# Optimization experiments

Measured on AMD Instinct MI355X. Metric: run time of the kernel, lower is better.

Reference implementation:

```python
import jax, jax.numpy as jnp
import numpy as np
import math

B, L, D, H = 2, 2048, 1024, 16
DK = D // H


def setup_inputs() -> dict:
    key = jax.random.key(0)
    ks = jax.random.split(key, 11)
    s = 1.0 / math.sqrt(D)
    inp = {
        "query": jax.random.normal(ks[0], (B, L, D), jnp.float32),
        "key": jax.random.normal(ks[1], (B, L, D), jnp.float32),
        "value": jax.random.normal(ks[2], (B, L, D), jnp.float32),
        # mask == True (==1) means masked-out; causal mask over future positions
        "mask": jnp.triu(jnp.ones((L, L), dtype=bool), k=1),
        "Wq": jax.random.normal(ks[3], (D, D), jnp.float32) * s,
        "bq": jnp.zeros((D,), jnp.float32),
        "Wk": jax.random.normal(ks[4], (D, D), jnp.float32) * s,
        "bk": jnp.zeros((D,), jnp.float32),
        "Wv": jax.random.normal(ks[5], (D, D), jnp.float32) * s,
        "bv": jnp.zeros((D,), jnp.float32),
        "Wo": jax.random.normal(ks[6], (D, D), jnp.float32) * s,
        "bo": jnp.zeros((D,), jnp.float32),
    }
    return inp


def reference(query, key, value, mask, Wq, bq, Wk, bk, Wv, bv, Wo, bo):
    # Linear projections, then split heads: [B, L, D] -> [B, H, L, DK]
    def proj(x, W, b):
        return (x @ W.T + b).reshape(B, -1, H, DK).transpose(0, 2, 1, 3)

    Q = proj(query, Wq, bq)
    K = proj(key, Wk, bk)
    V = proj(value, Wv, bv)

    scale = 1.0 / math.sqrt(DK)
    scores = jnp.einsum("bhqd,bhkd->bhqk", Q, K) * scale  # [B,H,Lq,Lk]
    scores = jnp.where(mask, -jnp.inf, scores)
    attn = jax.nn.softmax(scores, axis=-1)  # dropout p=0 (eval mode)
    out = jnp.einsum("bhqk,bhkd->bhqd", attn, V)
    out = out.transpose(0, 2, 1, 3).reshape(B, -1, D)  # merge heads
    return out @ Wo.T + bo
```

## Files before the change

### kernel.cpp

```cpp
#include <hip/hip_runtime.h>
#include <hip/hip_bf16.h>
#include <math.h>

#define NL 2048
#define ND 1024

typedef __attribute__((ext_vector_type(8))) __bf16 bf16x8;
typedef __attribute__((ext_vector_type(4))) float f32x4;
typedef __attribute__((ext_vector_type(16))) float f32x16;
typedef __attribute__((ext_vector_type(4))) short short4v;
typedef __attribute__((ext_vector_type(2))) unsigned uint2v;
typedef __attribute__((ext_vector_type(4))) unsigned uint4v;

__device__ __forceinline__ short f2bf(float f) {
    union { float f; unsigned u; } v; v.f = f;
    unsigned u = v.u;
    u += 0x7FFF + ((u >> 16) & 1);
    return (short)(u >> 16);
}

__device__ __forceinline__ unsigned cvtpk2(float lo, float hi) {
    unsigned r;
    asm("v_cvt_pk_bf16_f32 %0, %1, %2" : "=v"(r) : "v"(lo), "v"(hi));
    return r;
}

__device__ __forceinline__ void gload16(const short* g, short* l) {
    __builtin_amdgcn_global_load_lds(
        (const __attribute__((address_space(1))) void*)g,
        (__attribute__((address_space(3))) void*)l, 16, 0, 0);
}

__global__ __launch_bounds__(256) void cvt_f32_bf16_3(const float* __restrict__ a,
                                                      const float* __restrict__ b,
                                                      const float* __restrict__ c,
                                                      short* __restrict__ dst, int per) {
    const float* src = blockIdx.y == 0 ? a : blockIdx.y == 1 ? b : c;
    short* d = dst + (size_t)blockIdx.y * per;
    int i = (blockIdx.x * 256 + threadIdx.x) * 8;
    if (i < per) {
        f32x4 v0 = *(const f32x4*)&src[i];
        f32x4 v1 = *(const f32x4*)&src[i + 4];
        uint4v u = { cvtpk2(v0[0], v0[1]), cvtpk2(v0[2], v0[3]),
                     cvtpk2(v1[0], v1[1]), cvtpk2(v1[2], v1[3]) };
        *(uint4v*)&d[i] = u;
    }
}

__global__ __launch_bounds__(256) void gemm_qkv(
    const float* __restrict__ Xq, const float* __restrict__ Xk, const float* __restrict__ Xv,
    const short* __restrict__ Wqb, const short* __restrict__ Wkb, const short* __restrict__ Wvb,
    const float* __restrict__ bq, const float* __restrict__ bk, const float* __restrict__ bv,
    short* __restrict__ oq, short* __restrict__ ok, short* __restrict__ ov) {
    __shared__ alignas(16) short As[2][128 * 32];
    __shared__ alignas(16) short Bs[2][128 * 32];

    const int bid  = blockIdx.x;
    const int xcd  = bid & 7, slot = bid >> 3;
    const int panel = xcd * 12 + (slot >> 3);
    const int z    = panel >> 5;
    const int m0   = (panel & 31) * 128;
    const int n0   = (slot & 7) * 128;

    const float* X  = z == 0 ? Xq : z == 1 ? Xk : Xv;
    const short* Wb = z == 0 ? Wqb : z == 1 ? Wkb : Wvb;
    const float* bi = z == 0 ? bq : z == 1 ? bk : bv;
    short* outp     = z == 0 ? oq : z == 1 ? ok : ov;
    const float scl = z == 0 ? 0.125f * 1.44269504088896f : 1.0f;

    const int tid = threadIdx.x, lane = tid & 63, w = tid >> 6;
    const int wr = w >> 1, wc = w & 1, lr = lane >> 4, lc = lane & 15;

    const short* gB = &Wb[(n0 + w * 16 + (lane >> 2)) * 1024 + (lane & 3) * 8];
    const float* gA = &X[(m0 + (tid >> 3)) * 1024 + (tid & 7) * 4];
    const int arow = tid >> 3, acol = (tid & 7) * 4;

    f32x4 acc[4][4] = {};
    f32x4 av[4];

    #pragma unroll
    for (int p = 0; p < 4; ++p) av[p] = *(const f32x4*)&gA[p * 32 * 1024];
    gload16(gB, &Bs[0][w * 512]);
    gload16(gB + 64 * 1024, &Bs[0][w * 512 + 2048]);
    #pragma unroll
    for (int p = 0; p < 4; ++p) {
        uint2v uu = { cvtpk2(av[p][0], av[p][1]), cvtpk2(av[p][2], av[p][3]) };
        *(uint2v*)&As[0][(p * 32 + arow) * 32 + acol] = uu;
    }
    __syncthreads();

    int cur = 0;
    for (int t = 0; t < 32; ++t) {
        const int k1 = (t + 1) * 32;
        if (t < 31) {
            #pragma unroll
            for (int p = 0; p < 4; ++p)
                av[p] = *(const f32x4*)&gA[p * 32 * 1024 + k1];
            gload16(gB + k1, &Bs[cur ^ 1][w * 512]);
            gload16(gB + 64 * 1024 + k1, &Bs[cur ^ 1][w * 512 + 2048]);
        }

        bf16x8 a[4], b[4];
        #pragma unroll
        for (int mt = 0; mt < 4; ++mt)
            a[mt] = *(const bf16x8*)&As[cur][(wr * 64 + mt * 16 + lc) * 32 + lr * 8];
        #pragma unroll
        for (int nt = 0; nt < 4; ++nt)
            b[nt] = *(const bf16x8*)&Bs[cur][(wc * 64 + nt * 16 + lc) * 32 + lr * 8];
        __builtin_amdgcn_s_setprio(1);
        #pragma unroll
        for (int mt = 0; mt < 4; ++mt)
            #pragma unroll
            for (int nt = 0; nt < 4; ++nt)
                acc[mt][nt] = __builtin_amdgcn_mfma_f32_16x16x32_bf16(
                    a[mt], b[nt], acc[mt][nt], 0, 0, 0);
        __builtin_amdgcn_s_setprio(0);

        if (t < 31) {
            #pragma unroll
            for (int p = 0; p < 4; ++p) {
                uint2v uu = { cvtpk2(av[p][0], av[p][1]), cvtpk2(av[p][2], av[p][3]) };
                *(uint2v*)&As[cur ^ 1][(p * 32 + arow) * 32 + acol] = uu;
            }
        }
        __syncthreads();
        cur ^= 1;
    }

    #pragma unroll
    for (int mt = 0; mt < 4; ++mt)
        #pragma unroll
        for (int nt = 0; nt < 4; ++nt)
            #pragma unroll
            for (int r = 0; r < 4; ++r) {
                int grow = m0 + wr * 64 + mt * 16 + lr * 4 + r;
                int gcol = n0 + wc * 64 + nt * 16 + lc;
                float val = (acc[mt][nt][r] + bi[gcol]) * scl;
                int bh = (grow >> 11) * 16 + (gcol >> 6);
                int q  = grow & 2047;
                int dk = gcol & 63;
                size_t addr;
                if (z == 2)
                    addr = (size_t)bh * 131072 + (size_t)(q >> 6) * 4096 +
                           ((q >> 4) & 3) * 1024 + (dk >> 5) * 512 +
                           ((q >> 3) & 1) * 256 + (dk & 31) * 8 + (q & 7);
                else
                    addr = (size_t)bh * 131072 + (size_t)(q >> 5) * 2048 +
                           (dk >> 4) * 512 + ((dk >> 3) & 1) * 256 +
                           (q & 31) * 8 + (dk & 7);
                outp[addr] = f2bf(val);
            }
}

__global__ __launch_bounds__(256) void gemm_out(const short* __restrict__ Abf,
                                                const short* __restrict__ Wob,
                                                const float* __restrict__ bo,
                                                float* __restrict__ out) {
    __shared__ alignas(16) short As[2][128 * 32];
    __shared__ alignas(16) short Bs[2][128 * 32];

    const int bid = blockIdx.x;
    const int xcd = bid & 7, slot = bid >> 3;
    const int m0  = (xcd * 4 + (slot >> 3)) * 128;
    const int n0  = (slot & 7) * 128;

    const int tid = threadIdx.x, lane = tid & 63, w = tid >> 6;
    const int wr = w >> 1, wc = w & 1, lr = lane >> 4, lc = lane & 15;

    const short* gA = &Abf[(m0 + w * 16 + (lane >> 2)) * 1024 + (lane & 3) * 8];
    const short* gB = &Wob[(n0 + w * 16 + (lane >> 2)) * 1024 + (lane & 3) * 8];

    f32x4 acc[4][4] = {};

    gload16(gA, &As[0][w * 512]);
    gload16(gA + 64 * 1024, &As[0][w * 512 + 2048]);
    gload16(gB, &Bs[0][w * 512]);
    gload16(gB + 64 * 1024, &Bs[0][w * 512 + 2048]);
    __syncthreads();

    int cur = 0;
    for (int t = 0; t < 32; ++t) {
        const int k1 = (t + 1) * 32;
        if (t < 31) {
            gload16(gA + k1, &As[cur ^ 1][w * 512]);
            gload16(gA + 64 * 1024 + k1, &As[cur ^ 1][w * 512 + 2048]);
            gload16(gB + k1, &Bs[cur ^ 1][w * 512]);
            gload16(gB + 64 * 1024 + k1, &Bs[cur ^ 1][w * 512 + 2048]);
        }

        bf16x8 a[4], b[4];
        #pragma unroll
        for (int mt = 0; mt < 4; ++mt)
            a[mt] = *(const bf16x8*)&As[cur][(wr * 64 + mt * 16 + lc) * 32 + lr * 8];
        #pragma unroll
        for (int nt = 0; nt < 4; ++nt)
            b[nt] = *(const bf16x8*)&Bs[cur][(wc * 64 + nt * 16 + lc) * 32 + lr * 8];
        __builtin_amdgcn_s_setprio(1);
        #pragma unroll
        for (int mt = 0; mt < 4; ++mt)
            #pragma unroll
            for (int nt = 0; nt < 4; ++nt)
                acc[mt][nt] = __builtin_amdgcn_mfma_f32_16x16x32_bf16(
                    a[mt], b[nt], acc[mt][nt], 0, 0, 0);
        __builtin_amdgcn_s_setprio(0);
        __syncthreads();
        cur ^= 1;
    }

    #pragma unroll
    for (int mt = 0; mt < 4; ++mt)
        #pragma unroll
        for (int nt = 0; nt < 4; ++nt)
            #pragma unroll
            for (int r = 0; r < 4; ++r) {
                int grow = m0 + wr * 64 + mt * 16 + lr * 4 + r;
                int gcol = n0 + wc * 64 + nt * 16 + lc;
                out[grow * 1024 + gcol] = acc[mt][nt][r] + bo[gcol];
            }
}

__global__ __launch_bounds__(128, 3) void flash_attn(const short* __restrict__ Q,
                                                     const short* __restrict__ K,
                                                     const short* __restrict__ Vt,
                                                     short* __restrict__ AO) {
    __shared__ float mrg[64][49];

    const int tid  = threadIdx.x;
    const int lane = tid & 63;
    const int w    = tid >> 6;
    const int ql   = lane & 31;
    const int hi   = lane >> 5;

    const int bid  = blockIdx.x;
    const int xcd  = bid & 7;
    const int idx  = bid >> 3;
    const int bh   = xcd * 4 + (idx & 3);
    const int t    = 63 - (idx >> 2);
    const int q0   = t * 32;
    const int qa   = q0 + ql;
    const int nkb  = (t >> 1) + 1;
    const int nkb2 = nkb >> 1;
    const int kb_lo = w == 0 ? 0 : nkb2;
    const int kb_hi = w == 0 ? nkb2 : nkb;

    const short* Qp = Q  + (size_t)bh * 131072 + (size_t)t * 2048 + lane * 8;
    const short* Kp = K  + (size_t)bh * 131072 + lane * 8;
    const short* Vp = Vt + (size_t)bh * 131072 + lane * 8;

    bf16x8 qf[4];
    #pragma unroll
    for (int ks = 0; ks < 4; ++ks)
        qf[ks] = *(const bf16x8*)&Qp[ks * 512];

    f32x16 ot0 = {}, ot1 = {}, lacc = {};

    for (int kb = kb_lo; kb < kb_hi; ++kb) {
        bf16x8 kf[8];
        #pragma unroll
        for (int ks = 0; ks < 4; ++ks) {
            kf[2 * ks]     = *(const bf16x8*)&Kp[(size_t)(2 * kb) * 2048 + ks * 512];
            kf[2 * ks + 1] = *(const bf16x8*)&Kp[(size_t)(2 * kb + 1) * 2048 + ks * 512];
        }

        f32x16 st0 = {}, st1 = {};
        __builtin_amdgcn_s_setprio(1);
        #pragma unroll
        for (int ks = 0; ks < 4; ++ks) {
            st0 = __builtin_amdgcn_mfma_f32_32x32x16_bf16(kf[2 * ks],     qf[ks], st0, 0, 0, 0);
            st1 = __builtin_amdgcn_mfma_f32_32x32x16_bf16(kf[2 * ks + 1], qf[ks], st1, 0, 0, 0);
        }
        __builtin_amdgcn_s_setprio(0);

        bf16x8 vf[8];
        #pragma unroll
        for (int ks = 0; ks < 4; ++ks) {
            vf[2 * ks]     = *(const bf16x8*)&Vp[(size_t)kb * 4096 + ks * 1024];
            vf[2 * ks + 1] = *(const bf16x8*)&Vp[(size_t)kb * 4096 + ks * 1024 + 512];
        }

        if (kb == nkb - 1) {
            const int kv0 = kb * 64;
            #pragma unroll
            for (int r = 0; r < 16; ++r) {
                const int cr = (r & 3) + 8 * (r >> 2) + 4 * hi;
                if (kv0 + cr > qa)      st0[r] = -3.0e38f;
                if (kv0 + 32 + cr > qa) st1[r] = -3.0e38f;
            }
        }

        #pragma unroll
        for (int r = 0; r < 16; ++r) {
            st0[r] = exp2f(st0[r]);
            st1[r] = exp2f(st1[r]);
            lacc[r] += st0[r] + st1[r];
        }

        bf16x8 pf[4];
        #pragma unroll
        for (int blk = 0; blk < 2; ++blk) {
            const f32x16 s = blk ? st1 : st0;
            #pragma unroll
            for (int pks = 0; pks < 2; ++pks) {
                const int b = pks * 8;
                unsigned xa = cvtpk2(s[b + 0], s[b + 1]);
                unsigned xb = cvtpk2(s[b + 2], s[b + 3]);
                unsigned ya = cvtpk2(s[b + 4], s[b + 5]);
                unsigned yb = cvtpk2(s[b + 6], s[b + 7]);
                uint2v s0 = __builtin_amdgcn_permlane32_swap(xa, ya, false, false);
                uint2v s1 = __builtin_amdgcn_permlane32_swap(xb, yb, false, false);
                union { unsigned u[4]; bf16x8 v; } pu;
                pu.u[0] = s0[0]; pu.u[1] = s1[0]; pu.u[2] = s0[1]; pu.u[3] = s1[1];
                pf[blk * 2 + pks] = pu.v;
            }
        }

        __builtin_amdgcn_s_setprio(1);
        #pragma unroll
        for (int ks = 0; ks < 4; ++ks) {
            ot0 = __builtin_amdgcn_mfma_f32_32x32x16_bf16(vf[2 * ks],     pf[ks], ot0, 0, 0, 0);
            ot1 = __builtin_amdgcn_mfma_f32_32x32x16_bf16(vf[2 * ks + 1], pf[ks], ot1, 0, 0, 0);
        }
        __builtin_amdgcn_s_setprio(0);
    }

    if (w == 0) {
        #pragma unroll
        for (int r = 0; r < 16; ++r) {
            mrg[lane][r]      = ot0[r];
            mrg[lane][16 + r] = ot1[r];
            mrg[lane][32 + r] = lacc[r];
        }
    }
    __syncthreads();
    if (w == 1) {
        #pragma unroll
        for (int r = 0; r < 16; ++r) {
            ot0[r]  += mrg[lane][r];
            ot1[r]  += mrg[lane][16 + r];
            lacc[r] += mrg[lane][32 + r];
        }
        float sm[16];
        #pragma unroll
        for (int r = 0; r < 16; ++r) sm[r] = lacc[r];
        #pragma unroll
        for (int s = 8; s > 0; s >>= 1)
            #pragma unroll
            for (int i = 0; i < s; ++i) sm[i] += sm[i + s];
        const float l = sm[0] + __shfl_xor(sm[0], 32);
        const float inv = 1.f / l;

        const int b_ = bh >> 4, h_ = bh & 15;
        short* aoRow = AO + ((size_t)(b_ * NL + qa)) * ND + h_ * 64;
        #pragma unroll
        for (int db = 0; db < 2; ++db) {
            const f32x16 o = db ? ot1 : ot0;
            #pragma unroll
            for (int g = 0; g < 4; ++g) {
                short4v sv;
                #pragma unroll
                for (int i = 0; i < 4; ++i) sv[i] = f2bf(o[g * 4 + i] * inv);
                *(short4v*)&aoRow[db * 32 + g * 8 + 4 * hi] = sv;
            }
        }
    }
}

extern "C" void kernel_launch(void* const* d_in, const int* in_sizes, int n_in,
                              void* d_out, int out_size, void* d_ws, size_t ws_size,
                              hipStream_t stream) {
    const float* query = (const float*)d_in[0];
    const float* key   = (const float*)d_in[1];
    const float* value = (const float*)d_in[2];
    const float* Wq = (const float*)d_in[4];
    const float* bq = (const float*)d_in[5];
    const float* Wk = (const float*)d_in[6];
    const float* bk = (const float*)d_in[7];
    const float* Wv = (const float*)d_in[8];
    const float* bv = (const float*)d_in[9];
    const float* Wo = (const float*)d_in[10];
    const float* bo = (const float*)d_in[11];

    short* ws    = (short*)d_ws;
    short* q_ws  = ws;
    short* k_ws  = ws + (4 << 20);
    short* vt_ws = ws + (8 << 20);
    short* wbf   = ws + (12 << 20);
    short* ao_ws = ws + (12 << 20);
    short* wobf  = ws;

    cvt_f32_bf16_3<<<dim3(512, 3), 256, 0, stream>>>(Wq, Wk, Wv, wbf, 1 << 20);
    gemm_qkv<<<dim3(768), 256, 0, stream>>>(
        query, key, value,
        wbf, wbf + (1 << 20), wbf + (2 << 20),
        bq, bk, bv, q_ws, k_ws, vt_ws);
    flash_attn<<<dim3(2048), dim3(128), 0, stream>>>(q_ws, k_ws, vt_ws, ao_ws);
    cvt_f32_bf16_3<<<dim3(512, 1), 256, 0, stream>>>(Wo, Wo, Wo, wobf, 1 << 20);
    gemm_out<<<dim3(256), 256, 0, stream>>>(ao_ws, wobf, bo, (float*)d_out);
}
```

Before: 119.6 us.

## Deepen GEMM pipelines to triple/quad buffering with one barrier per k-step

The QKV projection GEMM moves from double to triple buffering and keeps two fp32 A prefetches in flight, using explicit vmcnt waits and a single raw s_barrier per k-step. The output GEMM moves to a four-stage LDS ring with loads issued two tiles ahead, also with one barrier per iteration. Both aim to hide global-load latency and drop the second __syncthreads per step. In exchange they use more LDS per block, which may reduce occupancy, and rely on hand-counted waitcnt values being correct.

```diff
diff --git a/kernel.cpp b/kernel.cpp
--- a/kernel.cpp
+++ b/kernel.cpp
@@ -52,8 +52,8 @@
     const short* __restrict__ Wqb, const short* __restrict__ Wkb, const short* __restrict__ Wvb,
     const float* __restrict__ bq, const float* __restrict__ bk, const float* __restrict__ bv,
     short* __restrict__ oq, short* __restrict__ ok, short* __restrict__ ov) {
-    __shared__ alignas(16) short As[2][128 * 32];
-    __shared__ alignas(16) short Bs[2][128 * 32];
+    __shared__ alignas(16) short As[3][4096];
+    __shared__ alignas(16) short Bs[3][4096];
 
     const int bid  = blockIdx.x;
     const int xcd  = bid & 7, slot = bid >> 3;
@@ -76,55 +76,109 @@
     const int arow = tid >> 3, acol = (tid & 7) * 4;
 
     f32x4 acc[4][4] = {};
-    f32x4 av[4];
-
-    #pragma unroll
-    for (int p = 0; p < 4; ++p) av[p] = *(const f32x4*)&gA[p * 32 * 1024];
+    f32x4 avE[4], avO[4];
+
+    #pragma unroll
+    for (int p = 0; p < 4; ++p) avE[p] = *(const f32x4*)&gA[p * 32768];
+    #pragma unroll
+    for (int p = 0; p < 4; ++p) avO[p] = *(const f32x4*)&gA[p * 32768 + 32];
     gload16(gB, &Bs[0][w * 512]);
-    gload16(gB + 64 * 1024, &Bs[0][w * 512 + 2048]);
+    gload16(gB + 65536, &Bs[0][w * 512 + 2048]);
     #pragma unroll
     for (int p = 0; p < 4; ++p) {
-        uint2v uu = { cvtpk2(av[p][0], av[p][1]), cvtpk2(av[p][2], av[p][3]) };
+        uint2v uu = { cvtpk2(avE[p][0], avE[p][1]), cvtpk2(avE[p][2], avE[p][3]) };
         *(uint2v*)&As[0][(p * 32 + arow) * 32 + acol] = uu;
     }
-    __syncthreads();
-
-    int cur = 0;
-    for (int t = 0; t < 32; ++t) {
-        const int k1 = (t + 1) * 32;
-        if (t < 31) {
-            #pragma unroll
-            for (int p = 0; p < 4; ++p)
-                av[p] = *(const f32x4*)&gA[p * 32 * 1024 + k1];
-            gload16(gB + k1, &Bs[cur ^ 1][w * 512]);
-            gload16(gB + 64 * 1024 + k1, &Bs[cur ^ 1][w * 512 + 2048]);
-        }
-
+
+#define QKV_STEP(T, RD, WT, AVL, AVW)                                          \
+    {                                                                          \
+        const int k2 = ((T) + 2) * 32, k1 = ((T) + 1) * 32;                    \
+        _Pragma("unroll")                                                      \
+        for (int p = 0; p < 4; ++p)                                            \
+            AVL[p] = *(const f32x4*)&gA[p * 32768 + k2];                       \
+        gload16(gB + k1, &Bs[WT][w * 512]);                                    \
+        gload16(gB + 65536 + k1, &Bs[WT][w * 512 + 2048]);                     \
+        asm volatile("s_waitcnt vmcnt(6)" ::: "memory");                       \
+        _Pragma("unroll")                                                      \
+        for (int p = 0; p < 4; ++p) {                                          \
+            uint2v uu = { cvtpk2(AVW[p][0], AVW[p][1]),                        \
+                          cvtpk2(AVW[p][2], AVW[p][3]) };                      \
+            *(uint2v*)&As[WT][(p * 32 + arow) * 32 + acol] = uu;               \
+        }                                                                      \
+        asm volatile("s_waitcnt lgkmcnt(0)" ::: "memory");                     \
+        __builtin_amdgcn_s_barrier();                                          \
+        asm volatile("" ::: "memory");                                         \
+        bf16x8 a[4], b[4];                                                     \
+        _Pragma("unroll")                                                      \
+        for (int mt = 0; mt < 4; ++mt)                                         \
+            a[mt] = *(const bf16x8*)&As[RD][(wr * 64 + mt * 16 + lc) * 32 + lr * 8]; \
+        _Pragma("unroll")                                                      \
+        for (int nt = 0; nt < 4; ++nt)                                         \
+            b[nt] = *(const bf16x8*)&Bs[RD][(wc * 64 + nt * 16 + lc) * 32 + lr * 8]; \
+        __builtin_amdgcn_s_setprio(1);                                         \
+        _Pragma("unroll")                                                      \
+        for (int mt = 0; mt < 4; ++mt)                                         \
+            _Pragma("unroll")                                                  \
+            for (int nt = 0; nt < 4; ++nt)                                     \
+                acc[mt][nt] = __builtin_amdgcn_mfma_f32_16x16x32_bf16(         \
+                    a[mt], b[nt], acc[mt][nt], 0, 0, 0);                       \
+        __builtin_amdgcn_s_setprio(0);                                         \
+    }
+
+    int rd = 0;
+    for (int t = 0; t < 30; t += 2) {
+        const int wt0 = rd + 1 == 3 ? 0 : rd + 1;
+        QKV_STEP(t, rd, wt0, avE, avO);
+        const int rd1 = wt0;
+        const int wt1 = rd1 + 1 == 3 ? 0 : rd1 + 1;
+        QKV_STEP(t + 1, rd1, wt1, avO, avE);
+        rd = wt1;
+    }
+#undef QKV_STEP
+
+    {
+        gload16(gB + 31 * 32, &Bs[1][w * 512]);
+        gload16(gB + 65536 + 31 * 32, &Bs[1][w * 512 + 2048]);
+        asm volatile("s_waitcnt vmcnt(2)" ::: "memory");
+        #pragma unroll
+        for (int p = 0; p < 4; ++p) {
+            uint2v uu = { cvtpk2(avO[p][0], avO[p][1]), cvtpk2(avO[p][2], avO[p][3]) };
+            *(uint2v*)&As[1][(p * 32 + arow) * 32 + acol] = uu;
+        }
+        asm volatile("s_waitcnt lgkmcnt(0)" ::: "memory");
+        __builtin_amdgcn_s_barrier();
+        asm volatile("" ::: "memory");
         bf16x8 a[4], b[4];
         #pragma unroll
         for (int mt = 0; mt < 4; ++mt)
-            a[mt] = *(const bf16x8*)&As[cur][(wr * 64 + mt * 16 + lc) * 32 + lr * 8];
-        #pragma unroll
-        for (int nt = 0; nt < 4; ++nt)
-            b[nt] = *(const bf16x8*)&Bs[cur][(wc * 64 + nt * 16 + lc) * 32 + lr * 8];
-        __builtin_amdgcn_s_setprio(1);
+            a[mt] = *(const bf16x8*)&As[0][(wr * 64 + mt * 16 + lc) * 32 + lr * 8];
+        #pragma unroll
+        for (int nt = 0; nt < 4; ++nt)
+            b[nt] = *(const bf16x8*)&Bs[0][(wc * 64 + nt * 16 + lc) * 32 + lr * 8];
         #pragma unroll
         for (int mt = 0; mt < 4; ++mt)
             #pragma unroll
             for (int nt = 0; nt < 4; ++nt)
                 acc[mt][nt] = __builtin_amdgcn_mfma_f32_16x16x32_bf16(
                     a[mt], b[nt], acc[mt][nt], 0, 0, 0);
-        __builtin_amdgcn_s_setprio(0);
-
-        if (t < 31) {
-            #pragma unroll
-            for (int p = 0; p < 4; ++p) {
-                uint2v uu = { cvtpk2(av[p][0], av[p][1]), cvtpk2(av[p][2], av[p][3]) };
-                *(uint2v*)&As[cur ^ 1][(p * 32 + arow) * 32 + acol] = uu;
-            }
-        }
-        __syncthreads();
-        cur ^= 1;
+    }
+    {
+        asm volatile("s_waitcnt vmcnt(0)" ::: "memory");
+        __builtin_amdgcn_s_barrier();
+        asm volatile("" ::: "memory");
+        bf16x8 a[4], b[4];
+        #pragma unroll
+        for (int mt = 0; mt < 4; ++mt)
+            a[mt] = *(const bf16x8*)&As[1][(wr * 64 + mt * 16 + lc) * 32 + lr * 8];
+        #pragma unroll
+        for (int nt = 0; nt < 4; ++nt)
+            b[nt] = *(const bf16x8*)&Bs[1][(wc * 64 + nt * 16 + lc) * 32 + lr * 8];
+        #pragma unroll
+        for (int mt = 0; mt < 4; ++mt)
+            #pragma unroll
+            for (int nt = 0; nt < 4; ++nt)
+                acc[mt][nt] = __builtin_amdgcn_mfma_f32_16x16x32_bf16(
+                    a[mt], b[nt], acc[mt][nt], 0, 0, 0);
     }
 
     #pragma unroll
@@ -156,8 +210,8 @@
                                                 const short* __restrict__ Wob,
                                                 const float* __restrict__ bo,
                                                 float* __restrict__ out) {
-    __shared__ alignas(16) short As[2][128 * 32];
-    __shared__ alignas(16) short Bs[2][128 * 32];
+    __shared__ alignas(16) short As[4][4096];
+    __shared__ alignas(16) short Bs[4][4096];
 
     const int bid = blockIdx.x;
     const int xcd = bid & 7, slot = bid >> 3;
@@ -172,29 +226,33 @@
 
     f32x4 acc[4][4] = {};
 
-    gload16(gA, &As[0][w * 512]);
-    gload16(gA + 64 * 1024, &As[0][w * 512 + 2048]);
-    gload16(gB, &Bs[0][w * 512]);
-    gload16(gB + 64 * 1024, &Bs[0][w * 512 + 2048]);
-    __syncthreads();
-
-    int cur = 0;
-    for (int t = 0; t < 32; ++t) {
-        const int k1 = (t + 1) * 32;
-        if (t < 31) {
-            gload16(gA + k1, &As[cur ^ 1][w * 512]);
-            gload16(gA + 64 * 1024 + k1, &As[cur ^ 1][w * 512 + 2048]);
-            gload16(gB + k1, &Bs[cur ^ 1][w * 512]);
-            gload16(gB + 64 * 1024 + k1, &Bs[cur ^ 1][w * 512 + 2048]);
-        }
+    gload16(gA,         &As[0][w * 512]);
+    gload16(gA + 65536, &As[0][w * 512 + 2048]);
+    gload16(gB,         &Bs[0][w * 512]);
+    gload16(gB + 65536, &Bs[0][w * 512 + 2048]);
+    gload16(gA + 32,         &As[1][w * 512]);
+    gload16(gA + 65536 + 32, &As[1][w * 512 + 2048]);
+    gload16(gB + 32,         &Bs[1][w * 512]);
+    gload16(gB + 65536 + 32, &Bs[1][w * 512 + 2048]);
+
+    for (int t = 0; t < 30; ++t) {
+        const int ws_ = (t + 2) & 3, rd = t & 3;
+        const int k2 = (t + 2) * 32;
+        gload16(gA + k2,         &As[ws_][w * 512]);
+        gload16(gA + 65536 + k2, &As[ws_][w * 512 + 2048]);
+        gload16(gB + k2,         &Bs[ws_][w * 512]);
+        gload16(gB + 65536 + k2, &Bs[ws_][w * 512 + 2048]);
+        asm volatile("s_waitcnt vmcnt(8)" ::: "memory");
+        __builtin_amdgcn_s_barrier();
+        asm volatile("" ::: "memory");
 
         bf16x8 a[4], b[4];
         #pragma unroll
         for (int mt = 0; mt < 4; ++mt)
-            a[mt] = *(const bf16x8*)&As[cur][(wr * 64 + mt * 16 + lc) * 32 + lr * 8];
-        #pragma unroll
-        for (int nt = 0; nt < 4; ++nt)
-            b[nt] = *(const bf16x8*)&Bs[cur][(wc * 64 + nt * 16 + lc) * 32 + lr * 8];
+            a[mt] = *(const bf16x8*)&As[rd][(wr * 64 + mt * 16 + lc) * 32 + lr * 8];
+        #pragma unroll
+        for (int nt = 0; nt < 4; ++nt)
+            b[nt] = *(const bf16x8*)&Bs[rd][(wc * 64 + nt * 16 + lc) * 32 + lr * 8];
         __builtin_amdgcn_s_setprio(1);
         #pragma unroll
         for (int mt = 0; mt < 4; ++mt)
@@ -203,8 +261,27 @@
                 acc[mt][nt] = __builtin_amdgcn_mfma_f32_16x16x32_bf16(
                     a[mt], b[nt], acc[mt][nt], 0, 0, 0);
         __builtin_amdgcn_s_setprio(0);
-        __syncthreads();
-        cur ^= 1;
+    }
+    #pragma unroll
+    for (int pt = 0; pt < 2; ++pt) {
+        if (pt == 0) asm volatile("s_waitcnt vmcnt(4)" ::: "memory");
+        else         asm volatile("s_waitcnt vmcnt(0)" ::: "memory");
+        __builtin_amdgcn_s_barrier();
+        asm volatile("" ::: "memory");
+        const int rd = 2 + pt;
+        bf16x8 a[4], b[4];
+        #pragma unroll
+        for (int mt = 0; mt < 4; ++mt)
+            a[mt] = *(const bf16x8*)&As[rd][(wr * 64 + mt * 16 + lc) * 32 + lr * 8];
+        #pragma unroll
+        for (int nt = 0; nt < 4; ++nt)
+            b[nt] = *(const bf16x8*)&Bs[rd][(wc * 64 + nt * 16 + lc) * 32 + lr * 8];
+        #pragma unroll
+        for (int mt = 0; mt < 4; ++mt)
+            #pragma unroll
+            for (int nt = 0; nt < 4; ++nt)
+                acc[mt][nt] = __builtin_amdgcn_mfma_f32_16x16x32_bf16(
+                    a[mt], b[nt], acc[mt][nt], 0, 0, 0);
     }
 
     #pragma unroll
```

After: 128.5 us. 1.07x slower.
